# Optimization experiments

Hardware: AMD Instinct MI355X
Metric: run time of the kernel (lower is better)

Reference implementation:

```python
import jax, jax.numpy as jnp
import numpy as np

B, T, N, D, M, H, L, FF = 8, 128, 24, 128, 9, 8, 4, 1024
F = D // H          # spatial head dim = 16
HD = D // H         # temporal head dim = 16
ND = N * D          # 3072
NM = N * M          # 216


def setup_inputs() -> dict:
    key = jax.random.key(0)
    ks = jax.random.split(key, 24)
    w = lambda k, shape, s=0.05: (jax.random.normal(k, shape, jnp.float32) * s)
    z = lambda shape: jnp.zeros(shape, jnp.float32)
    return {
        "inputs": jax.random.normal(ks[0], (B, T, NM), jnp.float32),
        "emb_W": w(ks[1], (N, M, D)), "emb_b": z((N, D)),
        "sp_Wq": w(ks[2], (L, H, N, D, F)), "sp_bq": z((L, H, N, F)),
        "sp_Wk": w(ks[3], (L, H, D, F)), "sp_bk": z((L, H, F)),
        "sp_Wv": w(ks[4], (L, H, D, F)), "sp_bv": z((L, H, F)),
        "tmp_Win": w(ks[5], (L, N, 3 * D, D)), "tmp_bin": z((L, N, 3 * D)),
        "tmp_Wout": w(ks[6], (L, N, D, D)), "tmp_bout": z((L, N, D)),
        "ff_W1": w(ks[7], (L, ND, FF)), "ff_b1": z((L, FF)),
        "ff_W2": w(ks[8], (L, FF, ND)), "ff_b2": z((L, ND)),
        "ln_g": jnp.ones((L, ND), jnp.float32), "ln_b": z((L, ND)),
        "fin_W": w(ks[9], (ND, NM)), "fin_b": z((NM,)),
    }


def _ln(x, g, b):
    m = jnp.mean(x, -1, keepdims=True)
    v = jnp.mean(jnp.square(x - m), -1, keepdims=True)
    return (x - m) * jax.lax.rsqrt(v + 1e-5) * g + b


def _pos_encoding():
    # standard sinusoidal PE; original adds it over the FIRST axis of the
    # (B, T, N*D) tensor (applied before the permute), so index by B.
    pos = jnp.arange(B, dtype=jnp.float32)[:, None]
    div = jnp.exp(jnp.arange(0, ND, 2, dtype=jnp.float32) * (-np.log(10000.0) / ND))
    pe = jnp.zeros((B, ND), jnp.float32)
    pe = pe.at[:, 0::2].set(jnp.sin(pos * div)).at[:, 1::2].set(jnp.cos(pos * div))
    return pe


def reference(inputs, emb_W, emb_b, sp_Wq, sp_bq, sp_Wk, sp_bk, sp_Wv, sp_bv,
              tmp_Win, tmp_bin, tmp_Wout, tmp_bout, ff_W1, ff_b1, ff_W2, ff_b2,
              ln_g, ln_b, fin_W, fin_b):
    # joint embedding: (B,T,N,M) @ (N,M,D) -> (B,T,N,D)
    x4 = inputs.reshape(B, T, N, M)
    emb = (jnp.einsum('btnm,nmd->btnd', x4, emb_W) + emb_b).reshape(B, T, ND)
    emb = emb + _pos_encoding()[:, None, :]
    h = emb.transpose(1, 0, 2)                     # (T, B, ND)
    # PyTorch float attn_mask is ADDED to scores: +1.0 strictly below diagonal
    mask = jnp.tril(jnp.ones((T, T), jnp.float32), -1)
    for l in range(L):
        xr = h.reshape(T, B, N, D)
        # ---- spatial attention (shared K/V, per-joint Q, per head) ----
        k = jnp.einsum('tbnd,hdf->tbhnf', xr, sp_Wk[l]) + sp_bk[l][:, None, :]
        v = jnp.einsum('tbnd,hdf->tbhnf', xr, sp_Wv[l]) + sp_bv[l][:, None, :]
        q = jnp.einsum('tbnd,hndf->tbhnf', xr, sp_Wq[l]) + sp_bq[l]
        a = jax.nn.softmax(jnp.einsum('tbhnf,tbhmf->tbhnm', q, k) / jnp.sqrt(jnp.float32(F)), -1)
        sp = jnp.einsum('tbhnm,tbhmf->tbhnf', a, v)
        sp = sp.transpose(0, 1, 3, 2, 4).reshape(T, B, ND)   # joint-major, heads concat within joint
        sp = _ln(sp + h, ln_g[l], ln_b[l])
        # ---- temporal attention (per-joint nn.MultiheadAttention) ----
        Wq_t, Wk_t, Wv_t = tmp_Win[l, :, :D], tmp_Win[l, :, D:2 * D], tmp_Win[l, :, 2 * D:]
        bq_t, bk_t, bv_t = tmp_bin[l, :, :D], tmp_bin[l, :, D:2 * D], tmp_bin[l, :, 2 * D:]
        qt = (jnp.einsum('tbnd,ned->tbne', xr, Wq_t) + bq_t).reshape(T, B, N, H, HD)
        kt = (jnp.einsum('tbnd,ned->tbne', xr, Wk_t) + bk_t).reshape(T, B, N, H, HD)
        vt = (jnp.einsum('tbnd,ned->tbne', xr, Wv_t) + bv_t).reshape(T, B, N, H, HD)
        st = jnp.einsum('tbnhe,sbnhe->bnhts', qt, kt) / jnp.sqrt(jnp.float32(HD)) + mask
        at = jax.nn.softmax(st, -1)
        ot = jnp.einsum('bnhts,sbnhe->tbnhe', at, vt).reshape(T, B, N, D)
        tp = (jnp.einsum('tbnd,nod->tbno', ot, tmp_Wout[l]) + tmp_bout[l]).reshape(T, B, ND)
        tp = _ln(tp + h, ln_g[l], ln_b[l])
        # ---- FFN (no activation in original) + residual + shared LN ----
        a2 = sp + tp
        o = (a2 @ ff_W1[l] + ff_b1[l]) @ ff_W2[l] + ff_b2[l]
        h = _ln(o + a2, ln_g[l], ln_b[l])
    out = h @ fin_W + fin_b                        # (T, B, NM)
    return out.transpose(1, 0, 2) + inputs
```

## Files before the change

kernel.cpp:

```cpp
#include <hip/hip_runtime.h>
#include <hip/hip_bf16.h>
#include <math.h>

constexpr int kB = 8, kT = 128, kN = 24, kD = 128, kM = 9, kH = 8, kL = 4, kFF = 1024;
constexpr int kF = 16;
constexpr int kHD = 16;
constexpr int kND = kN * kD;
constexpr int kNM = kN * kM;
constexpr int kP = kB * kT;

using bf16x8 = __attribute__((ext_vector_type(8))) short;
using f32x4  = __attribute__((ext_vector_type(4))) float;
typedef __hip_bfloat16 bf16;

__device__ __forceinline__ void load_lds16(const void* g, void* l) {
  __builtin_amdgcn_global_load_lds(
      (const __attribute__((address_space(1))) void*)g,
      (__attribute__((address_space(3))) void*)l, 16, 0, 0);
}

template<int BM, int BN, bool OUTBF>
__global__ __launch_bounds__(256) void mfma_gemm(
    const bf16* __restrict__ A, const bf16* __restrict__ Bm,
    const float* __restrict__ bias, void* __restrict__ Cv,
    int M, int Nc, int K, int ldB, int sAi, int sCi,
    long offAg, long offBg, long offCg, int sBg)
{
  constexpr int WM = BM / 2, WN = BN / 2;
  constexpr int MT = WM / 16, NT = WN / 16;
  constexpr int ASLOTS = BM * 8;
  constexpr int BSLOTS = BN * 8;
  constexpr int CSTR = BN + 4;
  __shared__ __align__(16) char smem[(BM + BN) * 64 * 2];
  bf16* As = (bf16*)smem;
  bf16* Bs = (bf16*)(smem + BM * 64 * 2);
  float* Cs = (float*)smem;

  int g = blockIdx.z;
  A  += offAg * g;
  Bm += offBg * g;
  long cbase = offCg * (long)g;
  int bOff = sBg * g;

  int m0 = blockIdx.y * BM, n0 = blockIdx.x * BN;
  int tid = threadIdx.x, lane = tid & 63, wave = tid >> 6;
  int wm = wave >> 1, wn = wave & 1;
  int fr = lane & 15, fq = lane >> 4;

  f32x4 acc[MT][NT] = {};

  for (int kk = 0; kk < K; kk += 64) {
#pragma unroll
    for (int s = tid; s < ASLOTS; s += 256) {
      int m = s >> 3, kq = (s & 7) ^ (m & 7);
      load_lds16(A + (size_t)(m0 + m) * sAi + (kk + kq * 8), &As[s * 8]);
    }
#pragma unroll
    for (int s = tid; s < BSLOTS; s += 256) {
      int n = s >> 3, kq = (s & 7) ^ (n & 7);
      int nr = n0 + n; if (nr > Nc - 1) nr = Nc - 1;
      load_lds16(Bm + (size_t)nr * ldB + (kk + kq * 8), &Bs[s * 8]);
    }
    __syncthreads();
#pragma unroll
    for (int ks = 0; ks < 2; ks++) {
      bf16x8 af[MT], bfr[NT];
#pragma unroll
      for (int i = 0; i < MT; i++) {
        int row = wm * WM + i * 16 + fr;
        af[i] = *(const bf16x8*)&As[row * 64 + (((ks * 4 + fq) ^ (row & 7)) * 8)];
      }
#pragma unroll
      for (int j = 0; j < NT; j++) {
        int row = wn * WN + j * 16 + fr;
        bfr[j] = *(const bf16x8*)&Bs[row * 64 + (((ks * 4 + fq) ^ (row & 7)) * 8)];
      }
#pragma unroll
      for (int i = 0; i < MT; i++)
#pragma unroll
        for (int j = 0; j < NT; j++)
          acc[i][j] = __builtin_amdgcn_mfma_f32_16x16x32_bf16(af[i], bfr[j], acc[i][j], 0, 0, 0);
    }
    __syncthreads();
  }

  constexpr int NCHUNK = BN / 16;
  int tcol = tid & (NCHUNK - 1);
  int trow = tid / NCHUNK;
  int colbase = n0 + tcol * 16;
  float vb[16];
  if (trow < 32) {
#pragma unroll
    for (int jj = 0; jj < 16; jj++)
      vb[jj] = bias ? bias[bOff + colbase + jj] : 0.f;
  }
#pragma unroll
  for (int i = 0; i < MT; i++) {
    __syncthreads();
#pragma unroll
    for (int j = 0; j < NT; j++)
#pragma unroll
      for (int r = 0; r < 4; r++)
        Cs[(wm * 16 + fq * 4 + r) * CSTR + wn * WN + j * 16 + fr] = acc[i][j][r];
    __syncthreads();
    if (trow < 32) {
      int row = m0 + (trow >> 4) * WM + i * 16 + (trow & 15);
      float vals[16];
#pragma unroll
      for (int jj = 0; jj < 4; jj++)
        *(float4*)&vals[jj * 4] = *(const float4*)&Cs[trow * CSTR + tcol * 16 + jj * 4];
#pragma unroll
      for (int jj = 0; jj < 16; jj++) vals[jj] += vb[jj];
      if (OUTBF) {
        bf16* cp = (bf16*)Cv + cbase + (size_t)row * sCi + colbase;
        union { bf16 h[8]; uint4 v; } pk;
#pragma unroll
        for (int half = 0; half < 2; half++) {
          if (colbase + half * 8 + 8 <= Nc) {
#pragma unroll
            for (int jj = 0; jj < 8; jj++) pk.h[jj] = __float2bfloat16(vals[half * 8 + jj]);
            *(uint4*)(cp + half * 8) = pk.v;
          }
        }
      } else {
        float* cp = (float*)Cv + cbase + (size_t)row * sCi + colbase;
#pragma unroll
        for (int jj = 0; jj < 4; jj++)
          if (colbase + jj * 4 + 4 <= Nc) *(float4*)(cp + jj * 4) = *(float4*)&vals[jj * 4];
      }
    }
  }
}

constexpr int NB_EMB = kP;
constexpr int NB_SPQ = kL * kH * kN;
constexpr int NB_SPK = kL * kH * kN;
constexpr int NB_SPV = kL * kH * kN;
constexpr int NB_TMP = (kL * kN * 384 * kD / 8) / 256;
constexpr int NB_CVT = (kL * 24 * 128 * 128 / 8) / 256;
constexpr int NB_SPB = (kL * 24 * 768) / 256;
constexpr int NB_W1  = (kFF / 64) * (kND / 64) * kL;
constexpr int NB_W2  = (kND / 64) * (kFF / 64) * kL;
constexpr int NB_FIN = ((kNM + 63) / 64) * (kND / 64);
constexpr int OFF_SPQ = NB_EMB;
constexpr int OFF_SPK = OFF_SPQ + NB_SPQ;
constexpr int OFF_SPV = OFF_SPK + NB_SPK;
constexpr int OFF_TMP = OFF_SPV + NB_SPV;
constexpr int OFF_CVT = OFF_TMP + NB_TMP;
constexpr int OFF_SPB = OFF_CVT + NB_CVT;
constexpr int OFF_W1  = OFF_SPB + NB_SPB;
constexpr int OFF_W2  = OFF_W1 + NB_W1;
constexpr int OFF_FIN = OFF_W2 + NB_W2;
constexpr int NB_PREP = OFF_FIN + NB_FIN;

__device__ __forceinline__ void trans_cvt_body(
    const float* __restrict__ in, bf16* __restrict__ out,
    int R, int C, int bx, int by, float (*t)[65], int tid)
{
  int c0 = bx * 64, r0 = by * 64;
  for (int s = tid; s < 1024; s += 256) {
    int rr = s >> 4, c4 = (s & 15) * 4;
    int r = r0 + rr, c = c0 + c4;
    float4 v;
    if (c + 4 <= C) v = *(const float4*)&in[(size_t)r * C + c];
    else {
      float tmp[4];
#pragma unroll
      for (int j = 0; j < 4; j++) tmp[j] = (c + j < C) ? in[(size_t)r * C + c + j] : 0.f;
      v = *(float4*)tmp;
    }
    *(float4*)&t[rr][c4] = v;
  }
  __syncthreads();
  for (int s = tid; s < 512; s += 256) {
    int cc = s >> 3, r8 = (s & 7) * 8;
    int c = c0 + cc;
    if (c < C) {
      union { bf16 h[8]; uint4 v; } pk;
#pragma unroll
      for (int j = 0; j < 8; j++) pk.h[j] = __float2bfloat16(t[r8 + j][cc]);
      *(uint4*)&out[(size_t)c * R + r0 + r8] = pk.v;
    }
  }
}

__device__ __forceinline__ void spw_transpose_body(
    const float* __restrict__ src, bf16* __restrict__ dst, float* ts, int tid)
{
  for (int s = tid; s < 512; s += 256) {
    float4 v = ((const float4*)src)[s];
    int d = s >> 2, f4 = (s & 3) * 4;
    ts[(f4 + 0) * 132 + d] = v.x;
    ts[(f4 + 1) * 132 + d] = v.y;
    ts[(f4 + 2) * 132 + d] = v.z;
    ts[(f4 + 3) * 132 + d] = v.w;
  }
  __syncthreads();
  int f = tid >> 4, d8 = (tid & 15) * 8;
  float4 a = *(const float4*)&ts[f * 132 + d8];
  float4 b = *(const float4*)&ts[f * 132 + d8 + 4];
  union { bf16 h[8]; uint4 v; } pk;
  pk.h[0] = __float2bfloat16(a.x); pk.h[1] = __float2bfloat16(a.y);
  pk.h[2] = __float2bfloat16(a.z); pk.h[3] = __float2bfloat16(a.w);
  pk.h[4] = __float2bfloat16(b.x); pk.h[5] = __float2bfloat16(b.y);
  pk.h[6] = __float2bfloat16(b.z); pk.h[7] = __float2bfloat16(b.w);
  *(uint4*)&dst[(size_t)f * 128 + d8] = pk.v;
}

__global__ __launch_bounds__(256) void prep_kernel(
    const float* __restrict__ sp_Wq, const float* __restrict__ sp_Wk,
    const float* __restrict__ sp_Wv, const float* __restrict__ tmp_Win,
    bf16* __restrict__ spW,
    const float* __restrict__ tmp_Wout, bf16* __restrict__ toWb,
    const float* __restrict__ sp_bq, const float* __restrict__ sp_bk,
    const float* __restrict__ sp_bv, const float* __restrict__ tmp_bin,
    float* __restrict__ spbc,
    const float* __restrict__ ff_W1, bf16* __restrict__ W1t,
    const float* __restrict__ ff_W2, bf16* __restrict__ W2t,
    const float* __restrict__ fin_W, bf16* __restrict__ finWt,
    const float* __restrict__ inp, const float* __restrict__ emb_W,
    const float* __restrict__ emb_b, float* __restrict__ hb,
    bf16* __restrict__ hbb)
{
  __shared__ __align__(16) char sm[64 * 65 * 4];
  int bid = blockIdx.x, tid = threadIdx.x;

  if (bid < OFF_SPQ) {
    int p = bid;
    int t = p / kB, b = p % kB;
    float* xs = (float*)sm;
    if (tid < kNM)
      xs[tid] = inp[((size_t)b * kT + t) * kNM + tid];
    __syncthreads();
    const float c1 = -logf(10000.f) / (float)kND;
    for (int c4 = tid; c4 < kND / 4; c4 += 256) {
      int c = c4 * 4;
      int n = c >> 7, d = c & 127;
      float4 acc = *(const float4*)&emb_b[n * kD + d];
#pragma unroll
      for (int m = 0; m < kM; m++) {
        float xv = xs[n * kM + m];
        float4 w = *(const float4*)&emb_W[((size_t)(n * kM + m)) * kD + d];
        acc.x += xv * w.x; acc.y += xv * w.y; acc.z += xv * w.z; acc.w += xv * w.w;
      }
      float ang0 = (float)b * expf((float)c * c1);
      float ang1 = (float)b * expf((float)(c + 2) * c1);
      acc.x += sinf(ang0); acc.y += cosf(ang0);
      acc.z += sinf(ang1); acc.w += cosf(ang1);
      *(float4*)&hb[(size_t)p * kND + c] = acc;
      union { bf16 h4[4]; uint2 v; } pk;
      pk.h4[0] = __float2bfloat16(acc.x); pk.h4[1] = __float2bfloat16(acc.y);
      pk.h4[2] = __float2bfloat16(acc.z); pk.h4[3] = __float2bfloat16(acc.w);
      *(uint2*)&hbb[(size_t)p * kND + c] = pk.v;
    }
  } else if (bid < OFF_SPK) {
    int idx = bid - OFF_SPQ;
    int l = idx / 192, rem = idx % 192;
    int hh = rem / 24, n = rem % 24;
    const float* src = sp_Wq + ((((size_t)l * kH + hh) * kN + n)) * (kD * kF);
    bf16* dst = spW + (((size_t)(l * 24 + n)) * 768 + hh * 16) * 128;
    spw_transpose_body(src, dst, (float*)sm, tid);
  } else if (bid < OFF_SPV) {
    int idx = bid - OFF_SPK;
    int l = idx / 192, rem = idx % 192;
    int hh = rem / 24, n = rem % 24;
    const float* src = sp_Wk + (((size_t)l * kH + hh)) * (kD * kF);
    bf16* dst = spW + (((size_t)(l * 24 + n)) * 768 + 128 + hh * 16) * 128;
    spw_transpose_body(src, dst, (float*)sm, tid);
  } else if (bid < OFF_TMP) {
    int idx = bid - OFF_SPV;
    int l = idx / 192, rem = idx % 192;
    int hh = rem / 24, n = rem % 24;
    const float* src = sp_Wv + (((size_t)l * kH + hh)) * (kD * kF);
    bf16* dst = spW + (((size_t)(l * 24 + n)) * 768 + 256 + hh * 16) * 128;
    spw_transpose_body(src, dst, (float*)sm, tid);
  } else if (bid < OFF_CVT) {
    long j8 = ((long)(bid - OFF_TMP) * 256 + tid) * 8;
    long ln = j8 / 49152, rem = j8 % 49152;
    const float* src = &tmp_Win[ln * 49152 + rem];
    float4 v0 = *(const float4*)src, v1 = *(const float4*)(src + 4);
    union { bf16 h[8]; uint4 v; } pk;
    pk.h[0] = __float2bfloat16(v0.x); pk.h[1] = __float2bfloat16(v0.y);
    pk.h[2] = __float2bfloat16(v0.z); pk.h[3] = __float2bfloat16(v0.w);
    pk.h[4] = __float2bfloat16(v1.x); pk.h[5] = __float2bfloat16(v1.y);
    pk.h[6] = __float2bfloat16(v1.z); pk.h[7] = __float2bfloat16(v1.w);
    *(uint4*)&spW[ln * 98304 + 49152 + rem] = pk.v;
  } else if (bid < OFF_SPB) {
    int i8 = ((bid - OFF_CVT) * 256 + tid) * 8;
    float4 v0 = *(const float4*)(tmp_Wout + i8);
    float4 v1 = *(const float4*)(tmp_Wout + i8 + 4);
    union { bf16 h[8]; uint4 v; } pk;
    pk.h[0] = __float2bfloat16(v0.x); pk.h[1] = __float2bfloat16(v0.y);
    pk.h[2] = __float2bfloat16(v0.z); pk.h[3] = __float2bfloat16(v0.w);
    pk.h[4] = __float2bfloat16(v1.x); pk.h[5] = __float2bfloat16(v1.y);
    pk.h[6] = __float2bfloat16(v1.z); pk.h[7] = __float2bfloat16(v1.w);
    *(uint4*)(toWb + i8) = pk.v;
  } else if (bid < OFF_W1) {
    int i = (bid - OFF_SPB) * 256 + tid;
    int r = i % 768;
    int n = (i / 768) % 24;
    int l = i / (768 * 24);
    int hh = (r & 127) >> 4, f = r & 15;
    float v;
    if (r < 128)      v = sp_bq[(((size_t)l * kH + hh) * kN + n) * kF + f];
    else if (r < 256) v = sp_bk[((size_t)l * kH + hh) * kF + f];
    else if (r < 384) v = sp_bv[((size_t)l * kH + hh) * kF + f];
    else              v = tmp_bin[((size_t)l * kN + n) * 384 + (r - 384)];
    spbc[i] = v;
  } else if (bid < OFF_W2) {
    int id2 = bid - OFF_W1;
    int bz = id2 / (16 * 48);
    int rem = id2 % (16 * 48);
    trans_cvt_body(ff_W1 + (size_t)bz * kND * kFF, W1t + (size_t)bz * kFF * kND,
                   kND, kFF, rem % 16, rem / 16, (float(*)[65])sm, tid);
  } else if (bid < OFF_FIN) {
    int id2 = bid - OFF_W2;
    int bz = id2 / (48 * 16);
    int rem = id2 % (48 * 16);
    trans_cvt_body(ff_W2 + (size_t)bz * kFF * kND, W2t + (size_t)bz * kND * kFF,
                   kFF, kND, rem % 48, rem / 48, (float(*)[65])sm, tid);
  } else {
    int id2 = bid - OFF_FIN;
    trans_cvt_body(fin_W, finWt, kND, kNM, id2 % 4, id2 / 4, (float(*)[65])sm, tid);
  }
}

__global__ __launch_bounds__(192) void sp_attn_kernel(
    const bf16* __restrict__ qkv, float* __restrict__ out)
{
  int p = blockIdx.x;
  __shared__ float s[24 * 388];
  for (int i = threadIdx.x; i < 2304; i += 192) {
    int n = i / 96, c4 = (i % 96) * 4;
    ushort4 u = *(const ushort4*)((const ushort*)qkv + ((size_t)n * kP + p) * 768 + c4);
    float4 f;
    f.x = __bfloat162float(*(const bf16*)&u.x);
    f.y = __bfloat162float(*(const bf16*)&u.y);
    f.z = __bfloat162float(*(const bf16*)&u.z);
    f.w = __bfloat162float(*(const bf16*)&u.w);
    *(float4*)&s[n * 388 + c4] = f;
  }
  __syncthreads();
  int hh = threadIdx.x / 24, n = threadIdx.x % 24;
  const float4* qr = (const float4*)(s + n * 388 + hh * 16);
  float4 q0 = qr[0], q1 = qr[1], q2 = qr[2], q3 = qr[3];
  float sc[24];
  float mx = -1e30f;
#pragma unroll
  for (int m = 0; m < 24; m++) {
    const float4* kr = (const float4*)(s + m * 388 + 128 + hh * 16);
    float4 k0 = kr[0], k1 = kr[1], k2 = kr[2], k3 = kr[3];
    float d = q0.x * k0.x + q0.y * k0.y + q0.z * k0.z + q0.w * k0.w
            + q1.x * k1.x + q1.y * k1.y + q1.z * k1.z + q1.w * k1.w
            + q2.x * k2.x + q2.y * k2.y + q2.z * k2.z + q2.w * k2.w
            + q3.x * k3.x + q3.y * k3.y + q3.z * k3.z + q3.w * k3.w;
    d *= 0.25f;
    sc[m] = d;
    mx = fmaxf(mx, d);
  }
  float sum = 0.f;
#pragma unroll
  for (int m = 0; m < 24; m++) { float e = __expf(sc[m] - mx); sc[m] = e; sum += e; }
  float inv = 1.f / sum;
  float4 o0 = {0,0,0,0}, o1 = {0,0,0,0}, o2 = {0,0,0,0}, o3 = {0,0,0,0};
#pragma unroll
  for (int m = 0; m < 24; m++) {
    const float4* vr = (const float4*)(s + m * 388 + 256 + hh * 16);
    float4 v0 = vr[0], v1 = vr[1], v2 = vr[2], v3 = vr[3];
    float w = sc[m];
    o0.x += w * v0.x; o0.y += w * v0.y; o0.z += w * v0.z; o0.w += w * v0.w;
    o1.x += w * v1.x; o1.y += w * v1.y; o1.z += w * v1.z; o1.w += w * v1.w;
    o2.x += w * v2.x; o2.y += w * v2.y; o2.z += w * v2.z; o2.w += w * v2.w;
    o3.x += w * v3.x; o3.y += w * v3.y; o3.z += w * v3.z; o3.w += w * v3.w;
  }
  float* orow = out + (size_t)p * kND + n * kD + hh * 16;
  o0.x *= inv; o0.y *= inv; o0.z *= inv; o0.w *= inv;
  o1.x *= inv; o1.y *= inv; o1.z *= inv; o1.w *= inv;
  o2.x *= inv; o2.y *= inv; o2.z *= inv; o2.w *= inv;
  o3.x *= inv; o3.y *= inv; o3.z *= inv; o3.w *= inv;
  *(float4*)(orow)      = o0;
  *(float4*)(orow + 4)  = o1;
  *(float4*)(orow + 8)  = o2;
  *(float4*)(orow + 12) = o3;
}

__global__ __launch_bounds__(128) void t_attn_mfma(
    const bf16* __restrict__ qkv, bf16* __restrict__ ot)
{
  int g = blockIdx.x;
  int hh = g & 7, n = (g >> 3) % 24, b = g / 192;
  __shared__ __align__(16) ushort Qs[128][40];
  __shared__ __align__(16) ushort Ks[128][40];
  __shared__ __align__(16) ushort Vt[16][136];
  __shared__ __align__(16) ushort Ps[128][136];

  for (int idx = threadIdx.x; idx < 256; idx += 128) {
    int t = idx >> 1, e8 = (idx & 1) * 8;
    const ushort* src = (const ushort*)qkv +
        ((size_t)n * kP + (size_t)t * kB + b) * 768 + 384 + hh * 16 + e8;
    uint4 q = *(const uint4*)(src);
    uint4 k = *(const uint4*)(src + 128);
    uint4 v = *(const uint4*)(src + 256);
    *(uint4*)&Qs[t][e8] = q;
    *(uint4*)&Ks[t][e8] = k;
    *(uint4*)&Qs[t][16 + e8] = make_uint4(0, 0, 0, 0);
    *(uint4*)&Ks[t][16 + e8] = make_uint4(0, 0, 0, 0);
    const ushort* vp = (const ushort*)&v;
#pragma unroll
    for (int j = 0; j < 8; j++) Vt[e8 + j][t] = vp[j];
  }
  __syncthreads();

  int lane = threadIdx.x & 63, w = threadIdx.x >> 6;
  int c = lane & 15, quad = lane >> 4;

  bf16x8 aq[4];
#pragma unroll
  for (int mt = 0; mt < 4; mt++)
    aq[mt] = *(const bf16x8*)&Qs[w * 64 + mt * 16 + c][quad * 8];
  f32x4 acc[4][8];
#pragma unroll
  for (int nt = 0; nt < 8; nt++) {
    bf16x8 bk = *(const bf16x8*)&Ks[nt * 16 + c][quad * 8];
#pragma unroll
    for (int mt = 0; mt < 4; mt++) {
      f32x4 z = {0.f, 0.f, 0.f, 0.f};
      acc[mt][nt] = __builtin_amdgcn_mfma_f32_16x16x32_bf16(aq[mt], bk, z, 0, 0, 0);
    }
  }

  f32x4 invv[4];
#pragma unroll
  for (int mt = 0; mt < 4; mt++) {
    int tbase = w * 64 + mt * 16 + quad * 4;
    f32x4 rm = {-1e30f, -1e30f, -1e30f, -1e30f};
#pragma unroll
    for (int nt = 0; nt < 8; nt++) {
      int s = nt * 16 + c;
#pragma unroll
      for (int r = 0; r < 4; r++) {
        float x = acc[mt][nt][r] * 0.25f + ((s < tbase + r) ? 1.f : 0.f);
        acc[mt][nt][r] = x;
        rm[r] = fmaxf(rm[r], x);
      }
    }
#pragma unroll
    for (int off = 1; off < 16; off <<= 1)
#pragma unroll
      for (int r = 0; r < 4; r++) rm[r] = fmaxf(rm[r], __shfl_xor(rm[r], off, 64));
    f32x4 rs = {0.f, 0.f, 0.f, 0.f};
#pragma unroll
    for (int nt = 0; nt < 8; nt++)
#pragma unroll
      for (int r = 0; r < 4; r++) {
        float pp = __expf(acc[mt][nt][r] - rm[r]);
        acc[mt][nt][r] = pp;
        rs[r] += pp;
      }
#pragma unroll
    for (int off = 1; off < 16; off <<= 1)
#pragma unroll
      for (int r = 0; r < 4; r++) rs[r] += __shfl_xor(rs[r], off, 64);
#pragma unroll
    for (int r = 0; r < 4; r++) invv[mt][r] = 1.f / rs[r];
#pragma unroll
    for (int nt = 0; nt < 8; nt++)
#pragma unroll
      for (int r = 0; r < 4; r++) {
        bf16 pb = __float2bfloat16(acc[mt][nt][r]);
        Ps[tbase + r][nt * 16 + c] = *(ushort*)&pb;
      }
  }

  f32x4 o[4] = {};
#pragma unroll
  for (int ks = 0; ks < 128; ks += 32) {
    bf16x8 bv = *(const bf16x8*)&Vt[c][ks + quad * 8];
#pragma unroll
    for (int mt = 0; mt < 4; mt++) {
      bf16x8 ap = *(const bf16x8*)&Ps[w * 64 + mt * 16 + c][ks + quad * 8];
      o[mt] = __builtin_amdgcn_mfma_f32_16x16x32_bf16(ap, bv, o[mt], 0, 0, 0);
    }
  }

#pragma unroll
  for (int mt = 0; mt < 4; mt++) {
#pragma unroll
    for (int r = 0; r < 4; r++) {
      int t = w * 64 + mt * 16 + quad * 4 + r;
      float val = o[mt][r] * invv[mt][r];
      ot[((size_t)n * kP + (size_t)t * kB + b) * 128 + hh * 16 + c] = __float2bfloat16(val);
    }
  }
}

__global__ __launch_bounds__(256) void fuse_a2_kernel(
    const float* __restrict__ sp, const float* __restrict__ tp,
    const float* __restrict__ h, const float* __restrict__ g,
    const float* __restrict__ be, float* __restrict__ a2, bf16* __restrict__ a2b)
{
  int row = blockIdx.x;
  const float4* s1p = (const float4*)(sp + (size_t)row * kND);
  const float4* s2p = (const float4*)(tp + (size_t)row * kND);
  const float4* hp  = (const float4*)(h  + (size_t)row * kND);
  float4 x1[3], x2[3];
  float sum1 = 0.f, sum2 = 0.f;
#pragma unroll
  for (int i = 0; i < 3; i++) {
    int c = threadIdx.x + 256 * i;
    float4 hv = hp[c], a = s1p[c], bb = s2p[c];
    a.x += hv.x; a.y += hv.y; a.z += hv.z; a.w += hv.w;
    bb.x += hv.x; bb.y += hv.y; bb.z += hv.z; bb.w += hv.w;
    x1[i] = a; x2[i] = bb;
    sum1 += a.x + a.y + a.z + a.w;
    sum2 += bb.x + bb.y + bb.z + bb.w;
  }
  __shared__ float red1[4], red2[4];
#pragma unroll
  for (int o = 32; o > 0; o >>= 1) { sum1 += __shfl_down(sum1, o, 64); sum2 += __shfl_down(sum2, o, 64); }
  int wid = threadIdx.x >> 6;
  if ((threadIdx.x & 63) == 0) { red1[wid] = sum1; red2[wid] = sum2; }
  __syncthreads();
  float mean1 = (red1[0] + red1[1] + red1[2] + red1[3]) * (1.f / kND);
  float mean2 = (red2[0] + red2[1] + red2[2] + red2[3]) * (1.f / kND);
  __syncthreads();
  float v1 = 0.f, v2 = 0.f;
#pragma unroll
  for (int i = 0; i < 3; i++) {
    float4 a = x1[i], bb = x2[i];
    v1 += (a.x - mean1) * (a.x - mean1) + (a.y - mean1) * (a.y - mean1)
        + (a.z - mean1) * (a.z - mean1) + (a.w - mean1) * (a.w - mean1);
    v2 += (bb.x - mean2) * (bb.x - mean2) + (bb.y - mean2) * (bb.y - mean2)
        + (bb.z - mean2) * (bb.z - mean2) + (bb.w - mean2) * (bb.w - mean2);
  }
#pragma unroll
  for (int o = 32; o > 0; o >>= 1) { v1 += __shfl_down(v1, o, 64); v2 += __shfl_down(v2, o, 64); }
  if ((threadIdx.x & 63) == 0) { red1[wid] = v1; red2[wid] = v2; }
  __syncthreads();
  float r1 = rsqrtf((red1[0] + red1[1] + red1[2] + red1[3]) * (1.f / kND) + 1e-5f);
  float r2 = rsqrtf((red2[0] + red2[1] + red2[2] + red2[3]) * (1.f / kND) + 1e-5f);
  const float4* g4 = (const float4*)g;
  const float4* b4 = (const float4*)be;
#pragma unroll
  for (int i = 0; i < 3; i++) {
    int c = threadIdx.x + 256 * i;
    float4 gc = g4[c], bc = b4[c];
    float4 a = x1[i], bb = x2[i], o;
    o.x = (a.x - mean1) * r1 * gc.x + bc.x + (bb.x - mean2) * r2 * gc.x + bc.x;
    o.y = (a.y - mean1) * r1 * gc.y + bc.y + (bb.y - mean2) * r2 * gc.y + bc.y;
    o.z = (a.z - mean1) * r1 * gc.z + bc.z + (bb.z - mean2) * r2 * gc.z + bc.z;
    o.w = (a.w - mean1) * r1 * gc.w + bc.w + (bb.w - mean2) * r2 * gc.w + bc.w;
    *(float4*)(a2 + (size_t)row * kND + c * 4) = o;
    union { bf16 h4[4]; uint2 v; } pk;
    pk.h4[0] = __float2bfloat16(o.x); pk.h4[1] = __float2bfloat16(o.y);
    pk.h4[2] = __float2bfloat16(o.z); pk.h4[3] = __float2bfloat16(o.w);
    *(uint2*)(a2b + (size_t)row * kND + c * 4) = pk.v;
  }
}

__global__ __launch_bounds__(256) void add_ln_dual_kernel(
    const float* __restrict__ a, const float* __restrict__ b,
    const float* __restrict__ g, const float* __restrict__ be,
    float* __restrict__ out, bf16* __restrict__ outb)
{
  int row = blockIdx.x;
  const float4* ar = (const float4*)(a + (size_t)row * kND);
  const float4* br = (const float4*)(b + (size_t)row * kND);
  float4 v[3];
  float s = 0.f;
#pragma unroll
  for (int i = 0; i < 3; i++) {
    int c = threadIdx.x + 256 * i;
    float4 x = ar[c], y = br[c];
    x.x += y.x; x.y += y.y; x.z += y.z; x.w += y.w;
    v[i] = x;
    s += x.x + x.y + x.z + x.w;
  }
  __shared__ float red[4];
#pragma unroll
  for (int o = 32; o > 0; o >>= 1) s += __shfl_down(s, o, 64);
  int wid = threadIdx.x >> 6;
  if ((threadIdx.x & 63) == 0) red[wid] = s;
  __syncthreads();
  float mean = (red[0] + red[1] + red[2] + red[3]) * (1.f / kND);
  __syncthreads();
  float vs = 0.f;
#pragma unroll
  for (int i = 0; i < 3; i++) {
    float4 x = v[i];
    vs += (x.x - mean) * (x.x - mean) + (x.y - mean) * (x.y - mean)
        + (x.z - mean) * (x.z - mean) + (x.w - mean) * (x.w - mean);
  }
#pragma unroll
  for (int o = 32; o > 0; o >>= 1) vs += __shfl_down(vs, o, 64);
  if ((threadIdx.x & 63) == 0) red[wid] = vs;
  __syncthreads();
  float rstd = rsqrtf((red[0] + red[1] + red[2] + red[3]) * (1.f / kND) + 1e-5f);
  const float4* g4 = (const float4*)g;
  const float4* b4 = (const float4*)be;
#pragma unroll
  for (int i = 0; i < 3; i++) {
    int c = threadIdx.x + 256 * i;
    float4 gc = g4[c], bc = b4[c], x = v[i], o;
    o.x = (x.x - mean) * rstd * gc.x + bc.x;
    o.y = (x.y - mean) * rstd * gc.y + bc.y;
    o.z = (x.z - mean) * rstd * gc.z + bc.z;
    o.w = (x.w - mean) * rstd * gc.w + bc.w;
    *(float4*)(out + (size_t)row * kND + c * 4) = o;
    union { bf16 h4[4]; uint2 v2; } pk;
    pk.h4[0] = __float2bfloat16(o.x); pk.h4[1] = __float2bfloat16(o.y);
    pk.h4[2] = __float2bfloat16(o.z); pk.h4[3] = __float2bfloat16(o.w);
    *(uint2*)(outb + (size_t)row * kND + c * 4) = pk.v2;
  }
}

__global__ __launch_bounds__(256) void ff1_reduce_kernel(
    const float* __restrict__ part, const float* __restrict__ bias,
    bf16* __restrict__ out)
{
  int i4 = (blockIdx.x * 256 + threadIdx.x) * 4;
  const size_t S = (size_t)kP * kFF;
  float4 p0 = *(const float4*)(part + i4);
  float4 p1 = *(const float4*)(part + S + i4);
  float4 p2 = *(const float4*)(part + 2 * S + i4);
  int col = i4 & (kFF - 1);
  float4 bb = *(const float4*)(bias + col);
  union { bf16 h4[4]; uint2 v; } pk;
  pk.h4[0] = __float2bfloat16(p0.x + p1.x + p2.x + bb.x);
  pk.h4[1] = __float2bfloat16(p0.y + p1.y + p2.y + bb.y);
  pk.h4[2] = __float2bfloat16(p0.z + p1.z + p2.z + bb.z);
  pk.h4[3] = __float2bfloat16(p0.w + p1.w + p2.w + bb.w);
  *(uint2*)(out + i4) = pk.v;
}

__global__ __launch_bounds__(256) void final_reduce_add_kernel(
    const float* __restrict__ part, const float* __restrict__ fin_b,
    const float* __restrict__ inp, float* __restrict__ out)
{
  int i = blockIdx.x * 256 + threadIdx.x;
  if (i >= kB * kT * kNM) return;
  int c = i % kNM;
  int rem = i / kNM;
  int t = rem % kT, b = rem / kT;
  size_t pi = (size_t)(t * kB + b) * kNM + c;
  const size_t S = (size_t)kP * kNM;
  float v = fin_b[c] + inp[i];
#pragma unroll
  for (int z = 0; z < 8; z++) v += part[z * S + pi];
  out[i] = v;
}

extern "C" void kernel_launch(void* const* d_in, const int* in_sizes, int n_in,
                              void* d_out, int out_size, void* d_ws, size_t ws_size,
                              hipStream_t stream)
{
  const float* inputs   = (const float*)d_in[0];
  const float* emb_W    = (const float*)d_in[1];
  const float* emb_b    = (const float*)d_in[2];
  const float* sp_Wq    = (const float*)d_in[3];
  const float* sp_bq    = (const float*)d_in[4];
  const float* sp_Wk    = (const float*)d_in[5];
  const float* sp_bk    = (const float*)d_in[6];
  const float* sp_Wv    = (const float*)d_in[7];
  const float* sp_bv    = (const float*)d_in[8];
  const float* tmp_Win  = (const float*)d_in[9];
  const float* tmp_bin  = (const float*)d_in[10];
  const float* tmp_Wout = (const float*)d_in[11];
  const float* tmp_bout = (const float*)d_in[12];
  const float* ff_W1    = (const float*)d_in[13];
  const float* ff_b1    = (const float*)d_in[14];
  const float* ff_W2    = (const float*)d_in[15];
  const float* ff_b2    = (const float*)d_in[16];
  const float* ln_g     = (const float*)d_in[17];
  const float* ln_b     = (const float*)d_in[18];
  const float* fin_W    = (const float*)d_in[19];
  const float* fin_b    = (const float*)d_in[20];
  float* out = (float*)d_out;

  char* wp = (char*)d_ws;
  size_t off = 0;
  auto alloc = [&](size_t bytes) { void* p = wp + off; off += (bytes + 255) & ~(size_t)255; return p; };
  bf16* spW   = (bf16*)alloc((size_t)kL * 24 * 768 * 128 * 2);
  bf16* toWb  = (bf16*)alloc((size_t)kL * 24 * 128 * 128 * 2);
  bf16* W1t   = (bf16*)alloc((size_t)kL * kFF * kND * 2);
  bf16* W2t   = (bf16*)alloc((size_t)kL * kND * kFF * 2);
  bf16* finWt = (bf16*)alloc((size_t)kNM * kND * 2);
  float* spbc = (float*)alloc((size_t)kL * 24 * 768 * 4);
  float* hb   = (float*)alloc((size_t)kP * kND * 4);
  bf16*  hbb  = (bf16*) alloc((size_t)kP * kND * 2);
  bf16*  qkvb = (bf16*) alloc((size_t)24 * kP * 768 * 2);
  float* sp   = (float*)alloc((size_t)kP * kND * 4);
  float* tp   = (float*)alloc((size_t)kP * kND * 4);
  float* a2   = (float*)alloc((size_t)kP * kND * 4);
  bf16*  a2b  = (bf16*) alloc((size_t)kP * kND * 2);
  bf16*  f1b  = (bf16*) alloc((size_t)kP * kFF * 2);
  bf16*  otb  = (bf16*) alloc((size_t)24 * kP * 128 * 2);
  float* ffpart  = sp;
  float* finpart = tp;

  prep_kernel<<<NB_PREP, 256, 0, stream>>>(
      sp_Wq, sp_Wk, sp_Wv, tmp_Win, spW,
      tmp_Wout, toWb,
      sp_bq, sp_bk, sp_bv, tmp_bin, spbc,
      ff_W1, W1t, ff_W2, W2t, fin_W, finWt,
      inputs, emb_W, emb_b, hb, hbb);

  for (int l = 0; l < kL; l++) {
    const float* lg = ln_g + (size_t)l * kND;
    const float* lb = ln_b + (size_t)l * kND;

    mfma_gemm<128, 128, true><<<dim3(6, 8, 24), 256, 0, stream>>>(
        hbb, spW + (size_t)l * 24 * 768 * 128, spbc + (size_t)l * 24 * 768, qkvb,
        kP, 768, 128, 128, kND, 768,
        128, 768 * 128, (long)kP * 768, 768);

    sp_attn_kernel<<<kP, 192, 0, stream>>>(qkvb, sp);
    t_attn_mfma<<<kB * 24 * 8, 128, 0, stream>>>(qkvb, otb);

    mfma_gemm<64, 64, false><<<dim3(2, 16, 24), 256, 0, stream>>>(
        otb, toWb + (size_t)l * 24 * 128 * 128, tmp_bout + (size_t)l * 24 * 128, tp,
        kP, 128, 128, 128, 128, kND,
        (long)kP * 128, 128 * 128, 128, 128);

    fuse_a2_kernel<<<kP, 256, 0, stream>>>(sp, tp, hb, lg, lb, a2, a2b);

    mfma_gemm<64, 64, false><<<dim3(kFF / 64, kP / 64, 3), 256, 0, stream>>>(
        a2b, W1t + (size_t)l * kFF * kND, nullptr, ffpart,
        kP, kFF, kND / 3, kND, kND, kFF,
        kND / 3, kND / 3, (long)kP * kFF, 0);
    ff1_reduce_kernel<<<(kP * kFF / 4) / 256, 256, 0, stream>>>(
        ffpart, ff_b1 + (size_t)l * kFF, f1b);

    mfma_gemm<64, 64, false><<<dim3(kND / 64, kP / 64, 1), 256, 0, stream>>>(
        f1b, W2t + (size_t)l * kND * kFF, ff_b2 + (size_t)l * kND, tp,
        kP, kND, kFF, kFF, kFF, kND, 0, 0, 0, 0);

    add_ln_dual_kernel<<<kP, 256, 0, stream>>>(tp, a2, lg, lb, hb, hbb);
  }

  mfma_gemm<64, 64, false><<<dim3((kNM + 63) / 64, kP / 64, 8), 256, 0, stream>>>(
      hbb, finWt, nullptr, finpart,
      kP, kNM, kND / 8, kND, kND, kNM,
      kND / 8, kND / 8, (long)kP * kNM, 0);
  final_reduce_add_kernel<<<(kB * kT * kNM + 255) / 256, 256, 0, stream>>>(
      finpart, fin_b, inputs, out);
}
```

Measured before the change: 774.4 us.

## Fuse FF1 split-K reduction into FF2 GEMM A-load and alias t_attn LDS

After: 844.1 us. 1.09x slower.

```diff
diff --git a/kernel.cpp b/kernel.cpp
--- a/kernel.cpp
+++ b/kernel.cpp
@@ -19,12 +19,14 @@
       (__attribute__((address_space(3))) void*)l, 16, 0, 0);
 }
 
-template<int BM, int BN, bool OUTBF>
+template<int BM, int BN, bool OUTBF, int AMODE = 0>
 __global__ __launch_bounds__(256) void mfma_gemm(
     const bf16* __restrict__ A, const bf16* __restrict__ Bm,
     const float* __restrict__ bias, void* __restrict__ Cv,
     int M, int Nc, int K, int ldB, int sAi, int sCi,
-    long offAg, long offBg, long offCg, int sBg)
+    long offAg, long offBg, long offCg, int sBg,
+    const float* __restrict__ aSrcF = nullptr,
+    const float* __restrict__ aBias = nullptr)
 {
   constexpr int WM = BM / 2, WN = BN / 2;
   constexpr int MT = WM / 16, NT = WN / 16;
@@ -50,10 +52,32 @@
   f32x4 acc[MT][NT] = {};
 
   for (int kk = 0; kk < K; kk += 64) {
-#pragma unroll
-    for (int s = tid; s < ASLOTS; s += 256) {
-      int m = s >> 3, kq = (s & 7) ^ (m & 7);
-      load_lds16(A + (size_t)(m0 + m) * sAi + (kk + kq * 8), &As[s * 8]);
+    if constexpr (AMODE == 1) {
+      const size_t SR = (size_t)kP * kFF;
+#pragma unroll
+      for (int s = tid; s < ASLOTS; s += 256) {
+        int m = s >> 3, kq = (s & 7) ^ (m & 7);
+        const float* p = aSrcF + (size_t)(m0 + m) * kFF + (kk + kq * 8);
+        union { bf16 h[8]; bf16x8 v; } pk;
+#pragma unroll
+        for (int j = 0; j < 8; j += 4) {
+          float4 p0 = *(const float4*)(p + j);
+          float4 p1 = *(const float4*)(p + SR + j);
+          float4 p2 = *(const float4*)(p + 2 * SR + j);
+          float4 bb = *(const float4*)(aBias + kk + kq * 8 + j);
+          pk.h[j + 0] = __float2bfloat16(p0.x + p1.x + p2.x + bb.x);
+          pk.h[j + 1] = __float2bfloat16(p0.y + p1.y + p2.y + bb.y);
+          pk.h[j + 2] = __float2bfloat16(p0.z + p1.z + p2.z + bb.z);
+          pk.h[j + 3] = __float2bfloat16(p0.w + p1.w + p2.w + bb.w);
+        }
+        *(bf16x8*)&As[s * 8] = pk.v;
+      }
+    } else {
+#pragma unroll
+      for (int s = tid; s < ASLOTS; s += 256) {
+        int m = s >> 3, kq = (s & 7) ^ (m & 7);
+        load_lds16(A + (size_t)(m0 + m) * sAi + (kk + kq * 8), &As[s * 8]);
+      }
     }
 #pragma unroll
     for (int s = tid; s < BSLOTS; s += 256) {
@@ -389,10 +413,11 @@
 {
   int g = blockIdx.x;
   int hh = g & 7, n = (g >> 3) % 24, b = g / 192;
-  __shared__ __align__(16) ushort Qs[128][40];
-  __shared__ __align__(16) ushort Ks[128][40];
-  __shared__ __align__(16) ushort Vt[16][136];
-  __shared__ __align__(16) ushort Ps[128][136];
+  __shared__ __align__(16) char smem[39168];
+  ushort (*Qs)[40]  = (ushort(*)[40])(smem);
+  ushort (*Ks)[40]  = (ushort(*)[40])(smem + 10240);
+  ushort (*Ps)[136] = (ushort(*)[136])(smem);
+  ushort (*Vt)[136] = (ushort(*)[136])(smem + 34816);
 
   for (int idx = threadIdx.x; idx < 256; idx += 128) {
     int t = idx >> 1, e8 = (idx & 1) * 8;
@@ -428,6 +453,7 @@
       acc[mt][nt] = __builtin_amdgcn_mfma_f32_16x16x32_bf16(aq[mt], bk, z, 0, 0, 0);
     }
   }
+  __syncthreads();
 
   f32x4 invv[4];
 #pragma unroll
@@ -612,25 +638,6 @@
     pk.h4[2] = __float2bfloat16(o.z); pk.h4[3] = __float2bfloat16(o.w);
     *(uint2*)(outb + (size_t)row * kND + c * 4) = pk.v2;
   }
-}
-
-__global__ __launch_bounds__(256) void ff1_reduce_kernel(
-    const float* __restrict__ part, const float* __restrict__ bias,
-    bf16* __restrict__ out)
-{
-  int i4 = (blockIdx.x * 256 + threadIdx.x) * 4;
-  const size_t S = (size_t)kP * kFF;
-  float4 p0 = *(const float4*)(part + i4);
-  float4 p1 = *(const float4*)(part + S + i4);
-  float4 p2 = *(const float4*)(part + 2 * S + i4);
-  int col = i4 & (kFF - 1);
-  float4 bb = *(const float4*)(bias + col);
-  union { bf16 h4[4]; uint2 v; } pk;
-  pk.h4[0] = __float2bfloat16(p0.x + p1.x + p2.x + bb.x);
-  pk.h4[1] = __float2bfloat16(p0.y + p1.y + p2.y + bb.y);
-  pk.h4[2] = __float2bfloat16(p0.z + p1.z + p2.z + bb.z);
-  pk.h4[3] = __float2bfloat16(p0.w + p1.w + p2.w + bb.w);
-  *(uint2*)(out + i4) = pk.v;
 }
 
 __global__ __launch_bounds__(256) void final_reduce_add_kernel(
@@ -693,7 +700,6 @@
   float* tp   = (float*)alloc((size_t)kP * kND * 4);
   float* a2   = (float*)alloc((size_t)kP * kND * 4);
   bf16*  a2b  = (bf16*) alloc((size_t)kP * kND * 2);
-  bf16*  f1b  = (bf16*) alloc((size_t)kP * kFF * 2);
   bf16*  otb  = (bf16*) alloc((size_t)24 * kP * 128 * 2);
   float* ffpart  = sp;
   float* finpart = tp;
@@ -728,12 +734,11 @@
         a2b, W1t + (size_t)l * kFF * kND, nullptr, ffpart,
         kP, kFF, kND / 3, kND, kND, kFF,
         kND / 3, kND / 3, (long)kP * kFF, 0);
-    ff1_reduce_kernel<<<(kP * kFF / 4) / 256, 256, 0, stream>>>(
-        ffpart, ff_b1 + (size_t)l * kFF, f1b);
-
-    mfma_gemm<64, 64, false><<<dim3(kND / 64, kP / 64, 1), 256, 0, stream>>>(
-        f1b, W2t + (size_t)l * kND * kFF, ff_b2 + (size_t)l * kND, tp,
-        kP, kND, kFF, kFF, kFF, kND, 0, 0, 0, 0);
+
+    mfma_gemm<64, 64, false, 1><<<dim3(kND / 64, kP / 64, 1), 256, 0, stream>>>(
+        nullptr, W2t + (size_t)l * kND * kFF, ff_b2 + (size_t)l * kND, tp,
+        kP, kND, kFF, kFF, 0, kND, 0, 0, 0, 0,
+        ffpart, ff_b1 + (size_t)l * kFF);
 
     add_ln_dual_kernel<<<kP, 256, 0, stream>>>(tp, a2, lg, lb, hb, hbb);
   }
```
